# Kernel optimization log

Hardware: AMD Instinct MI355X
Metric: run time of the kernel (lower is better)

Reference implementation:

```python
import jax, jax.numpy as jnp
import numpy as np

# static config (mirrors init_kwargs)
FS = 512          # frame_seqlen
NFPB = 2          # num_frame_per_block
NIB = 3           # num image/action/state blocks
NAPB = 32         # num_action_per_block
NSPB = 1          # num_state_per_block
LOCAL = 4         # local_attn_size (frames)
FIRST = FS
IMGB = NIB * NFPB * FS
ALEN = NIB * NAPB
SLEN = NIB * NSPB
TOTAL = FIRST + IMGB + ALEN + SLEN   # 3683
DIM = 1536
NH = 12
HD = DIM // NH    # 128
EPS = 1e-6


def _build_mask():
    # faithful port of _visualize_attention_mask (the block-sparse pattern)
    m = np.zeros((TOTAL, TOTAL), dtype=bool)
    fi0, fi1 = 0, FIRST
    ib0, ib1 = fi1, fi1 + IMGB
    a0, a1 = ib1, ib1 + ALEN
    s0 = a1
    m[fi0:fi1, fi0:fi1] = True  # first image: self only (sink)
    for b in range(NIB):
        bs = ib0 + b * NFPB * FS
        be = ib0 + (b + 1) * NFPB * FS
        m[bs:be, fi0:fi1] = True                      # sink
        kv = max(ib0, be - LOCAL * FS)                # local window
        m[bs:be, kv:be] = True
        m[bs:be, a0 + b * NAPB:a0 + (b + 1) * NAPB] = True
        m[bs:be, s0 + b * NSPB:s0 + (b + 1) * NSPB] = True
    for b in range(NIB):
        ab0 = a0 + b * NAPB
        ab1 = a0 + (b + 1) * NAPB
        m[ab0:ab1, fi0:fi1] = True
        ibe = ib0 + (b + 1) * NFPB * FS
        kv = max(ib0, ibe - LOCAL * FS)
        m[ab0:ab1, kv:ibe] = True
        m[ab0:ab1, ab0:ab1] = True
        m[ab0:ab1, s0 + b * NSPB:s0 + (b + 1) * NSPB] = True
    for b in range(NIB):
        ss = s0 + b * NSPB
        se = s0 + (b + 1) * NSPB
        m[ss:se, ss:se] = True
    return m

_MASK = jnp.asarray(_build_mask())


def _rms_norm(x, g):
    # WanRMSNorm over full dim, fp32 accumulation
    v = jnp.mean(jnp.square(x.astype(jnp.float32)), axis=-1, keepdims=True)
    return (x.astype(jnp.float32) * jax.lax.rsqrt(v + EPS)).astype(x.dtype) * g


def _rope(x, cos, sin):
    # x: [B,L,n,hd]; pairs are consecutive (..., hd//2, 2)
    B, L, n, d = x.shape
    xp = x.reshape(B, L, n, d // 2, 2)
    xr, xi = xp[..., 0], xp[..., 1]
    c = cos[None, :, None, :]
    s = sin[None, :, None, :]
    yr = xr * c - xi * s
    yi = xr * s + xi * c
    return jnp.stack([yr, yi], axis=-1).reshape(B, L, n, d)


def setup_inputs() -> dict:
    key = jax.random.key(0)
    ks = jax.random.split(key, 16)
    x = jax.random.normal(ks[0], (1, TOTAL, DIM), jnp.float32)

    def mkfreq(k, L):
        ang = jax.random.uniform(k, (L, HD // 2), jnp.float32, 0.0, 2.0 * np.pi)
        return jnp.stack([jnp.cos(ang), jnp.sin(ang)], axis=-1).reshape(L, HD)

    freqs = mkfreq(ks[1], FIRST + IMGB)
    freqs_action = mkfreq(ks[2], ALEN)
    freqs_state = mkfreq(ks[3], SLEN)
    sc = 1.0 / np.sqrt(DIM)
    Wq = jax.random.normal(ks[4], (DIM, DIM), jnp.float32) * sc
    Wk = jax.random.normal(ks[5], (DIM, DIM), jnp.float32) * sc
    Wv = jax.random.normal(ks[6], (DIM, DIM), jnp.float32) * sc
    Wo = jax.random.normal(ks[7], (DIM, DIM), jnp.float32) * sc
    bq = jax.random.normal(ks[8], (DIM,), jnp.float32) * 0.01
    bk = jax.random.normal(ks[9], (DIM,), jnp.float32) * 0.01
    bv = jax.random.normal(ks[10], (DIM,), jnp.float32) * 0.01
    bo = jax.random.normal(ks[11], (DIM,), jnp.float32) * 0.01
    gq = jnp.ones((DIM,), jnp.float32)
    gk = jnp.ones((DIM,), jnp.float32)
    return {"x": x, "freqs": freqs, "freqs_action": freqs_action,
            "freqs_state": freqs_state, "Wq": Wq, "bq": bq, "Wk": Wk, "bk": bk,
            "Wv": Wv, "bv": bv, "Wo": Wo, "bo": bo, "gq": gq, "gk": gk}


def reference(x, freqs, freqs_action, freqs_state, Wq, bq, Wk, bk, Wv, bv, Wo, bo, gq, gk):
    B, L, _ = x.shape
    q = _rms_norm(x @ Wq + bq, gq).reshape(B, L, NH, HD)
    k = _rms_norm(x @ Wk + bk, gk).reshape(B, L, NH, HD)
    v = (x @ Wv + bv).reshape(B, L, NH, HD)
    # full-sequence rope: image freqs then action freqs then state freqs
    f = jnp.concatenate([freqs, freqs_action, freqs_state], axis=0).reshape(L, HD // 2, 2)
    cos, sin = f[..., 0], f[..., 1]
    q = _rope(q, cos, sin)
    k = _rope(k, cos, sin)
    scores = jnp.einsum('bqnd,bknd->bnqk', q, k) / np.sqrt(HD)
    scores = jnp.where(_MASK[None, None], scores, jnp.finfo(scores.dtype).min)
    p = jax.nn.softmax(scores, axis=-1)
    o = jnp.einsum('bnqk,bknd->bqnd', p, v).reshape(B, L, DIM)
    return o @ Wo + bo
```

## Files before the change

### kernel.cpp

```cpp
#include <hip/hip_runtime.h>

#define LSEQ 3683
#define LPAD 3840
#define DIMSZ 1536
#define NHEAD 12
#define HEADD 128
#define SM_SCALE 0.088388347648318447f

typedef unsigned short u16;
typedef unsigned int u32;
typedef __bf16 bf16x8 __attribute__((ext_vector_type(8)));
typedef float f32x4 __attribute__((ext_vector_type(4)));

__device__ __forceinline__ u16 f2b(float f) {
  u32 u = __float_as_uint(f);
  u += 0x7FFFu + ((u >> 16) & 1u);
  return (u16)(u >> 16);
}
__device__ __forceinline__ float b2f(u16 s) {
  return __uint_as_float(((u32)s) << 16);
}
__device__ __forceinline__ int imax(int a, int b) { return a > b ? a : b; }

__device__ __forceinline__ void gl_lds16(const u16* g, u16* l) {
  __builtin_amdgcn_global_load_lds((const __attribute__((address_space(1))) u32*)g,
                                   (__attribute__((address_space(3))) u32*)l,
                                   16, 0, 0);
}

__device__ __forceinline__ int xcd_swz(int orig, int nwg) {
  int q = nwg >> 3, r = nwg & 7;
  int x = orig & 7, l = orig >> 3;
  return (x < r ? x * (q + 1) : r * (q + 1) + (x - r) * q) + l;
}

#define CONV_BLOCKS 5760
__global__ void prep_kernel(const float* __restrict__ x, u16* __restrict__ xb,
                            const float* __restrict__ W0, const float* __restrict__ W1,
                            const float* __restrict__ W2, const float* __restrict__ W3,
                            u16* __restrict__ Wt) {
  __shared__ float tile[32][33];
  int bx = blockIdx.x;
  if (bx < CONV_BLOCKS) {
    long idx = (long)bx * blockDim.x + threadIdx.x;
    long base = idx * 4;
    if (base >= (long)LPAD * DIMSZ) return;
    float4 v;
    if (base < (long)LSEQ * DIMSZ) v = *(const float4*)(x + base);
    else v = make_float4(0.f, 0.f, 0.f, 0.f);
    ushort4 o;
    o.x = f2b(v.x); o.y = f2b(v.y); o.z = f2b(v.z); o.w = f2b(v.w);
    *(ushort4*)(xb + base) = o;
  } else {
    int i = bx - CONV_BLOCKS;
    int z = i / 2304;
    int r = i % 2304;
    int bxx = r % 48, byy = r / 48;
    const float* W = (z == 0) ? W0 : (z == 1) ? W1 : (z == 2) ? W2 : W3;
    u16* dst = Wt + (size_t)z * DIMSZ * DIMSZ;
    int k0 = bxx * 32, n0 = byy * 32;
    int tx = threadIdx.x & 31, ty = threadIdx.x >> 5;
    #pragma unroll
    for (int q = 0; q < 4; q++) {
      int k = k0 + ty + q * 8;
      tile[ty + q * 8][tx] = W[(size_t)k * DIMSZ + n0 + tx];
    }
    __syncthreads();
    #pragma unroll
    for (int q = 0; q < 4; q++) {
      int n = n0 + ty + q * 8;
      dst[(size_t)n * DIMSZ + k0 + tx] = f2b(tile[tx][ty + q * 8]);
    }
  }
}

#define BAR() __builtin_amdgcn_s_barrier()
#define LGK0() asm volatile("s_waitcnt lgkmcnt(0)" ::: "memory")
#define LGK8() asm volatile("s_waitcnt lgkmcnt(8)" ::: "memory")
#define VMC9() asm volatile("s_waitcnt vmcnt(9)" ::: "memory")
#define VMC6() asm volatile("s_waitcnt vmcnt(6)" ::: "memory")
#define VMC3() asm volatile("s_waitcnt vmcnt(3)" ::: "memory")
#define VMC0() asm volatile("s_waitcnt vmcnt(0)" ::: "memory")
#define PRIO1() __builtin_amdgcn_s_setprio(1)
#define PRIO0() __builtin_amdgcn_s_setprio(0)

#define STG_A(buf, q, kt) \
  gl_lds16(gA + (size_t)((q) * 64) * DIMSZ + (kt), &Asg[buf][((q) * 64 + w * 8) * 64]);
#define STG_B(buf, q, kt) \
  gl_lds16(gB + (size_t)((q) * 64) * DIMSZ + (kt), &Bsg[buf][((q) * 64 + w * 8) * 64]);

#define LDA3(buf, mh) { \
  _Pragma("unroll") for (int mf = 0; mf < 3; mf++) { \
    int rb = (wm * 96 + (mh) * 48 + mf * 16) * 64; \
    Ar[mf * 2 + 0] = *(const bf16x8*)&Asg[buf][rb + off0]; \
    Ar[mf * 2 + 1] = *(const bf16x8*)&Asg[buf][rb + off1]; } }
#define LDB3(buf, nh) { \
  _Pragma("unroll") for (int nf = 0; nf < 3; nf++) { \
    int rb = (wn * 96 + (nh) * 48 + nf * 16) * 64; \
    Br[nh][nf * 2 + 0] = *(const bf16x8*)&Bsg[buf][rb + off0]; \
    Br[nh][nf * 2 + 1] = *(const bf16x8*)&Bsg[buf][rb + off1]; } }

#define MFMAQ3(mh, nh) { \
  _Pragma("unroll") for (int mf = 0; mf < 3; mf++) \
    _Pragma("unroll") for (int nf = 0; nf < 3; nf++) { \
      acc[(mh)*3+mf][(nh)*3+nf] = __builtin_amdgcn_mfma_f32_16x16x32_bf16(Ar[mf*2+0], Br[nh][nf*2+0], acc[(mh)*3+mf][(nh)*3+nf], 0, 0, 0); \
      acc[(mh)*3+mf][(nh)*3+nf] = __builtin_amdgcn_mfma_f32_16x16x32_bf16(Ar[mf*2+1], Br[nh][nf*2+1], acc[(mh)*3+mf][(nh)*3+nf], 0, 0, 0); } }

#define GEMM384_BODY() \
  STG_B(0, 0, 0) STG_B(0, 1, 0) STG_B(0, 2, 0) \
  STG_A(0, 0, 0) STG_A(0, 1, 0) STG_A(0, 2, 0) \
  STG_A(0, 3, 0) STG_A(0, 4, 0) STG_A(0, 5, 0) \
  STG_B(1, 0, 64) STG_B(1, 1, 64) STG_B(1, 2, 64) \
  STG_A(1, 0, 64) STG_A(1, 1, 64) STG_A(1, 2, 64) \
  STG_A(1, 3, 64) STG_A(1, 4, 64) STG_A(1, 5, 64) \
  VMC9(); \
  BAR(); \
  for (int i = 0; i < DIMSZ / 64 / 2 - 1; ++i) { \
    int kt2 = (2 * i + 2) * 64; \
    int kt3 = (2 * i + 3) * 64; \
    LDA3(0, 0) LDB3(0, 0) \
    LGK8(); BAR(); LGK0(); \
    PRIO1(); MFMAQ3(0, 0) PRIO0(); \
    BAR(); \
    LDB3(0, 1) \
    BAR(); LGK0(); \
    PRIO1(); MFMAQ3(0, 1) PRIO0(); \
    BAR(); \
    LDA3(0, 1) \
    STG_B(0, 0, kt2) STG_B(0, 1, kt2) STG_B(0, 2, kt2) \
    BAR(); LGK0(); \
    PRIO1(); MFMAQ3(1, 1) PRIO0(); \
    BAR(); \
    STG_A(0, 0, kt2) STG_A(0, 1, kt2) STG_A(0, 2, kt2) \
    VMC6(); BAR(); \
    PRIO1(); MFMAQ3(1, 0) PRIO0(); \
    BAR(); \
    LDA3(1, 0) LDB3(1, 0) \
    STG_A(0, 3, kt2) STG_A(0, 4, kt2) STG_A(0, 5, kt2) \
    LGK8(); BAR(); LGK0(); \
    PRIO1(); MFMAQ3(0, 0) PRIO0(); \
    BAR(); \
    LDB3(1, 1) \
    BAR(); LGK0(); \
    PRIO1(); MFMAQ3(0, 1) PRIO0(); \
    BAR(); \
    LDA3(1, 1) \
    STG_B(1, 0, kt3) STG_B(1, 1, kt3) STG_B(1, 2, kt3) \
    BAR(); LGK0(); \
    PRIO1(); MFMAQ3(1, 1) PRIO0(); \
    BAR(); \
    STG_A(1, 0, kt3) STG_A(1, 1, kt3) STG_A(1, 2, kt3) \
    STG_A(1, 3, kt3) STG_A(1, 4, kt3) STG_A(1, 5, kt3) \
    VMC9(); BAR(); \
    PRIO1(); MFMAQ3(1, 0) PRIO0(); \
    BAR(); \
  } \
  { \
    LDA3(0, 0) LDB3(0, 0) \
    LGK8(); BAR(); LGK0(); \
    PRIO1(); MFMAQ3(0, 0) PRIO0(); \
    BAR(); \
    LDB3(0, 1) \
    BAR(); LGK0(); \
    PRIO1(); MFMAQ3(0, 1) PRIO0(); \
    BAR(); \
    LDA3(0, 1) \
    BAR(); LGK0(); \
    PRIO1(); MFMAQ3(1, 1) PRIO0(); \
    BAR(); \
    VMC0(); BAR(); \
    PRIO1(); MFMAQ3(1, 0) PRIO0(); \
    BAR(); \
    LDA3(1, 0) LDB3(1, 0) \
    LGK8(); BAR(); LGK0(); \
    PRIO1(); MFMAQ3(0, 0) PRIO0(); \
    BAR(); \
    LDB3(1, 1) \
    BAR(); LGK0(); \
    PRIO1(); MFMAQ3(0, 1) PRIO0(); \
    BAR(); \
    LDA3(1, 1) \
    BAR(); LGK0(); \
    PRIO1(); MFMAQ3(1, 1) PRIO0(); \
    MFMAQ3(1, 0) \
  }

__launch_bounds__(512, 2)
__global__ void gemm_qkv384_kernel(const u16* __restrict__ A, const u16* __restrict__ Wt,
                                   const float* __restrict__ bq, const float* __restrict__ bk,
                                   const float* __restrict__ bv,
                                   u16* __restrict__ Qb, u16* __restrict__ Kb,
                                   u16* __restrict__ Vt) {
  __shared__ __align__(16) u16 Asg[2][384 * 64];
  __shared__ __align__(16) u16 Bsg[2][192 * 64];

  int wg = xcd_swz(blockIdx.x, 10 * 24);
  int nt = wg % 24;
  int m0 = (wg / 24) * 384;
  int which = nt >> 3;
  const float* bias = (which == 0) ? bq : (which == 1) ? bk : bv;

  int t = threadIdx.x;
  int lane = t & 63, w = t >> 6;
  int c = lane & 15, g = lane >> 4;
  int wm = w >> 1, wn = w & 1;

  int srow = t >> 3;
  int schunk = ((t & 7) ^ (srow & 7)) * 8;
  const u16* gA = A + (size_t)(m0 + srow) * DIMSZ + schunk;
  const u16* gB = Wt + (size_t)(nt * 192 + srow) * DIMSZ + schunk;

  int off0 = c * 64 + ((g) ^ (c & 7)) * 8;
  int off1 = c * 64 + ((g + 4) ^ (c & 7)) * 8;

  f32x4 acc[6][6];
  f32x4 zero = {0.f, 0.f, 0.f, 0.f};
  #pragma unroll
  for (int am = 0; am < 6; am++)
    #pragma unroll
    for (int an = 0; an < 6; an++) acc[am][an] = zero;
  bf16x8 Ar[6];
  bf16x8 Br[2][6];

  GEMM384_BODY()

  #pragma unroll
  for (int an = 0; an < 6; an++) {
    int ncol = (nt & 7) * 192 + wn * 96 + (an / 3) * 48 + (an % 3) * 16 + c;
    float bvv = bias[ncol];
    #pragma unroll
    for (int am = 0; am < 6; am++) {
      int rowb = m0 + wm * 96 + (am / 3) * 48 + (am % 3) * 16 + 4 * g;
      if (which == 2) {
        ushort4 pv;
        pv.x = f2b(acc[am][an][0] + bvv);
        pv.y = f2b(acc[am][an][1] + bvv);
        pv.z = f2b(acc[am][an][2] + bvv);
        pv.w = f2b(acc[am][an][3] + bvv);
        *(ushort4*)&Vt[(size_t)ncol * LPAD + rowb] = pv;
      } else {
        u16* P = (which == 1) ? Kb : Qb;
        #pragma unroll
        for (int r = 0; r < 4; r++)
          P[(size_t)(rowb + r) * DIMSZ + ncol] = f2b(acc[am][an][r] + bvv);
      }
    }
  }
}

#define LDB3S(buf) { \
  _Pragma("unroll") for (int nf = 0; nf < 3; nf++) { \
    int rb = (wn * 48 + nf * 16) * 64; \
    Br2[nf * 2 + 0] = *(const bf16x8*)&Bsg[buf][rb + off0]; \
    Br2[nf * 2 + 1] = *(const bf16x8*)&Bsg[buf][rb + off1]; } }

#define MFMAQ2(mh) { \
  _Pragma("unroll") for (int mf = 0; mf < 3; mf++) \
    _Pragma("unroll") for (int nf = 0; nf < 3; nf++) { \
      acc2[(mh)*3+mf][nf] = __builtin_amdgcn_mfma_f32_16x16x32_bf16(Ar[mf*2+0], Br2[nf*2+0], acc2[(mh)*3+mf][nf], 0, 0, 0); \
      acc2[(mh)*3+mf][nf] = __builtin_amdgcn_mfma_f32_16x16x32_bf16(Ar[mf*2+1], Br2[nf*2+1], acc2[(mh)*3+mf][nf], 0, 0, 0); } }

__launch_bounds__(512, 2)
__global__ void gemm_out192_kernel(const u16* __restrict__ A, const u16* __restrict__ Bt,
                                   const float* __restrict__ bias, float* __restrict__ outF) {
  __shared__ __align__(16) u16 Asg[2][192 * 64];
  __shared__ __align__(16) u16 Bsg[2][192 * 64];

  int wg = xcd_swz(blockIdx.x, 160);
  int nt = wg & 7;
  int m0 = (wg >> 3) * 192;

  int t = threadIdx.x;
  int lane = t & 63, w = t >> 6;
  int c = lane & 15, g = lane >> 4;
  int wm = w >> 2, wn = w & 3;

  int srow = t >> 3;
  int schunk = ((t & 7) ^ (srow & 7)) * 8;
  const u16* gA = A + (size_t)(m0 + srow) * DIMSZ + schunk;
  const u16* gB = Bt + (size_t)(nt * 192 + srow) * DIMSZ + schunk;

  int off0 = c * 64 + ((g) ^ (c & 7)) * 8;
  int off1 = c * 64 + ((g + 4) ^ (c & 7)) * 8;

  f32x4 acc2[6][3];
  f32x4 zero = {0.f, 0.f, 0.f, 0.f};
  #pragma unroll
  for (int am = 0; am < 6; am++)
    #pragma unroll
    for (int an = 0; an < 3; an++) acc2[am][an] = zero;
  bf16x8 Ar[6];
  bf16x8 Br2[6];

  STG_B(0, 0, 0) STG_B(0, 1, 0) STG_B(0, 2, 0)
  STG_A(0, 0, 0) STG_A(0, 1, 0) STG_A(0, 2, 0)
  STG_B(1, 0, 64) STG_B(1, 1, 64) STG_B(1, 2, 64)
  VMC3();
  BAR();

  for (int i = 0; i < DIMSZ / 64 / 2 - 1; ++i) {
    int ktn1 = (2 * i + 1) * 64;
    int kt2  = (2 * i + 2) * 64;
    int kt3  = (2 * i + 3) * 64;
    LDA3(0, 0) LDB3S(0)
    STG_A(1, 0, ktn1) STG_A(1, 1, ktn1) STG_A(1, 2, ktn1)
    LGK8(); BAR(); LGK0();
    PRIO1(); MFMAQ2(0) PRIO0();
    BAR();
    LDA3(0, 1)
    STG_B(0, 0, kt2) STG_B(0, 1, kt2) STG_B(0, 2, kt2)
    VMC3(); BAR(); LGK0();
    PRIO1(); MFMAQ2(1) PRIO0();
    BAR();
    LDA3(1, 0) LDB3S(1)
    STG_A(0, 0, kt2) STG_A(0, 1, kt2) STG_A(0, 2, kt2)
    LGK8(); BAR(); LGK0();
    PRIO1(); MFMAQ2(0) PRIO0();
    BAR();
    LDA3(1, 1)
    STG_B(1, 0, kt3) STG_B(1, 1, kt3) STG_B(1, 2, kt3)
    VMC3(); BAR(); LGK0();
    PRIO1(); MFMAQ2(1) PRIO0();
    BAR();
  }

  {
    LDA3(0, 0) LDB3S(0)
    STG_A(1, 0, DIMSZ - 64) STG_A(1, 1, DIMSZ - 64) STG_A(1, 2, DIMSZ - 64)
    LGK8(); BAR(); LGK0();
    PRIO1(); MFMAQ2(0) PRIO0();
    BAR();
    LDA3(0, 1)
    VMC0(); BAR(); LGK0();
    PRIO1(); MFMAQ2(1) PRIO0();
    BAR();
    LDA3(1, 0) LDB3S(1)
    LGK8(); BAR(); LGK0();
    PRIO1(); MFMAQ2(0) PRIO0();
    BAR();
    LDA3(1, 1)
    LGK0();
    MFMAQ2(1)
  }

  #pragma unroll
  for (int an = 0; an < 3; an++) {
    int ncol = nt * 192 + wn * 48 + an * 16 + c;
    float bvv = bias[ncol];
    #pragma unroll
    for (int am = 0; am < 6; am++) {
      int rowb = m0 + wm * 96 + (am / 3) * 48 + (am % 3) * 16 + 4 * g;
      #pragma unroll
      for (int r = 0; r < 4; r++) {
        int row = rowb + r;
        if (row < LSEQ) outF[(size_t)row * DIMSZ + ncol] = acc2[am][an][r] + bvv;
      }
    }
  }
}

__launch_bounds__(256)
__global__ void normrope_kernel(u16* __restrict__ Qb, u16* __restrict__ Kb,
                                const float* __restrict__ gq, const float* __restrict__ gk,
                                const float* __restrict__ freqs, const float* __restrict__ freqs_a,
                                const float* __restrict__ freqs_s) {
  int l = blockIdx.x;
  int sel = blockIdx.y;
  u16* P = sel ? Kb : Qb;
  const float* gvec = sel ? gk : gq;
  int t = threadIdx.x;
  u16* row = P + (size_t)l * DIMSZ;
  float xv[6];
  #pragma unroll
  for (int i = 0; i < 3; i++) {
    int p = i * 256 + t;
    ushort2 u = *(const ushort2*)(row + 2 * p);
    xv[2 * i] = b2f(u.x);
    xv[2 * i + 1] = b2f(u.y);
  }
  float ss = 0.f;
  #pragma unroll
  for (int i = 0; i < 6; i++) ss += xv[i] * xv[i];
  #pragma unroll
  for (int d = 32; d; d >>= 1) ss += __shfl_down(ss, d);
  __shared__ float red[4];
  __shared__ float rshare;
  if ((t & 63) == 0) red[t >> 6] = ss;
  __syncthreads();
  if (t == 0) rshare = rsqrtf((red[0] + red[1] + red[2] + red[3]) * (1.0f / DIMSZ) + 1e-6f);
  __syncthreads();
  float rms = rshare;

  const float* f = (l < 3584) ? (freqs + (size_t)l * HEADD)
                : (l < 3680) ? (freqs_a + (size_t)(l - 3584) * HEADD)
                             : (freqs_s + (size_t)(l - 3680) * HEADD);
  #pragma unroll
  for (int i = 0; i < 3; i++) {
    int p = i * 256 + t;
    int j = p & 63;
    float2 csn = *(const float2*)(f + 2 * j);
    float2 gv = *(const float2*)(gvec + 2 * p);
    float xr = xv[2 * i] * rms * gv.x;
    float xi = xv[2 * i + 1] * rms * gv.y;
    ushort2 o;
    o.x = f2b(xr * csn.x - xi * csn.y);
    o.y = f2b(xr * csn.y + xi * csn.x);
    *(ushort2*)(row + 2 * p) = o;
  }
}

#define PSLOT_U16 16640
#define NTAIL 84
__launch_bounds__(256, 2)
__global__ void attn_fused_kernel(const u16* __restrict__ Q, const u16* __restrict__ K,
                                  const u16* __restrict__ Vt, u16* __restrict__ O,
                                  u16* __restrict__ DP, float* __restrict__ Part) {
  __shared__ __align__(16) u16 Ks[2][32 * 136];
  __shared__ __align__(16) u16 Vs[2][128 * 40];
  __shared__ __align__(16) u16 Pl[4][32 * 40];

  int t = threadIdx.x, lane = t & 63, w = t >> 6, g = lane >> 4, c = lane & 15;
  const float c1 = SM_SCALE * 1.44269504088896340f;
  const float c2 = 12.0f * 1.44269504088896340f;

  f32x4 zero = {0.f, 0.f, 0.f, 0.f};
  bf16x8 onesv;
  {
    u16 ob = 0x3F80;
    #pragma unroll
    for (int i = 0; i < 8; i++) onesv[i] = ((const __bf16*)&ob)[0];
  }

  if (blockIdx.x < NTAIL) {
    char* smem = (char*)&Ks[0][0];
    float* Lsum = (float*)(smem + 20608);

    int j = blockIdx.x;
    int bxx = j % 7;
    int h = j / 7;
    int qt, part;
    if (bxx < 3) { qt = 112 + bxx; part = 0; }
    else if (bxx < 6) { qt = 112 + (bxx - 3); part = 1; }
    else { qt = 115; part = 0; }
    int qbase = qt * 32;
    bool heavy = (qt <= 114);

    int S0, E0, S1, E1, S2, E2, S3, E3, niv;
    if (qbase < 3680) {
      int b = (qbase - 3584) >> 5;
      int ibe = 512 + (b + 1) * 1024;
      int kv = imax(512, ibe - 2048);
      S0 = 0; E0 = 512; S1 = kv; E1 = ibe;
      S2 = 3584 + 32 * b; E2 = S2 + 32; S3 = 3680 + b; E3 = S3 + 1; niv = 4;
    } else {
      S0 = 3680; E0 = 3683; S1 = S2 = S3 = 0; E1 = E2 = E3 = 0; niv = 1;
    }
    bool diag = (qbase >= 3680);

    int B0 = S0 & ~31, B1 = S1 & ~31, B2 = S2 & ~31, B3 = S3 & ~31;
    int T1 = (E0 - B0 + 31) >> 5;
    int T2 = T1 + ((niv > 1) ? ((E1 - B1 + 31) >> 5) : 0);
    int T3 = T2 + ((niv > 2) ? ((E2 - B2 + 31) >> 5) : 0);
    int T4 = T3 + ((niv > 3) ? ((E3 - B3 + 31) >> 5) : 0);
    int ntile = T4;

    int rlo = 0, rhi = ntile;
    if (heavy) { int half = (ntile + 1) >> 1; if (part == 0) rhi = half; else rlo = half; }

    auto tile_of = [&](int f, int& k0, int& lo, int& hi) {
      k0 = B0 + (f << 5); lo = S0; hi = E0;
      if (niv > 1 && f >= T1) { k0 = B1 + ((f - T1) << 5); lo = S1; hi = E1; }
      if (niv > 2 && f >= T2) { k0 = B2 + ((f - T2) << 5); lo = S2; hi = E2; }
      if (niv > 3 && f >= T3) { k0 = B3 + ((f - T3) << 5); lo = S3; hi = E3; }
    };

    bf16x8 qf[2][4];
    #pragma unroll
    for (int a = 0; a < 2; a++) {
      const u16* qp = Q + (size_t)(qbase + a * 16 + c) * DIMSZ + h * HEADD + 8 * g;
      #pragma unroll
      for (int s = 0; s < 4; s++) qf[a][s] = *(const bf16x8*)(qp + 32 * s);
    }

    f32x4 acc[2][8];
    f32x4 lacc[2];
    #pragma unroll
    for (int a = 0; a < 2; a++) {
      lacc[a] = zero;
      #pragma unroll
      for (int cc = 0; cc < 8; cc++) acc[a][cc] = zero;
    }

    u16* PwA = (u16*)smem + w * 2560;
    u16* PwB = PwA + 1280;

    bf16x8 kc[2][4], vbuf[8], pa0, pa1;

    auto loadK = [&](int k0) {
      #pragma unroll
      for (int k2 = 0; k2 < 2; k2++) {
        const u16* kp = K + (size_t)(k0 + 16 * k2 + c) * DIMSZ + h * HEADD + 8 * g;
        #pragma unroll
        for (int s = 0; s < 4; s++) kc[k2][s] = *(const bf16x8*)(kp + 32 * s);
      }
    };
    auto loadV = [&](int k0) {
      #pragma unroll
      for (int cc = 0; cc < 8; cc++)
        vbuf[cc] = *(const bf16x8*)(Vt + (size_t)(h * HEADD + cc * 16 + c) * LPAD + k0 + 8 * g);
    };
    auto QKf = [&](f32x4 (&sc)[2][2]) {
      sc[0][0] = zero; sc[0][1] = zero; sc[1][0] = zero; sc[1][1] = zero;
      #pragma unroll
      for (int k2 = 0; k2 < 2; k2++)
        #pragma unroll
        for (int s = 0; s < 4; s++) {
          sc[0][k2] = __builtin_amdgcn_mfma_f32_16x16x32_bf16(qf[0][s], kc[k2][s], sc[0][k2], 0, 0, 0);
          sc[1][k2] = __builtin_amdgcn_mfma_f32_16x16x32_bf16(qf[1][s], kc[k2][s], sc[1][k2], 0, 0, 0);
        }
    };
    auto smstore = [&](f32x4 (&sc)[2][2], int k0, int lo, int hi, u16* Pw) {
      #pragma unroll
      for (int a = 0; a < 2; a++)
        #pragma unroll
        for (int k2 = 0; k2 < 2; k2++) {
          int k = k0 + k2 * 16 + c;
          bool valid = (k >= lo) && (k < hi);
          #pragma unroll
          for (int r = 0; r < 4; r++) {
            float p = __builtin_amdgcn_exp2f(sc[a][k2][r] * c1 - c2);
            bool v = valid;
            if (diag) { int qr = qbase + a * 16 + 4 * g + r; v = v && (k == qr); }
            Pw[(a * 16 + 4 * g + r) * 40 + k2 * 16 + c] = v ? f2b(p) : (u16)0;
          }
        }
    };
    auto readP = [&](u16* Pw) {
      pa0 = *(const bf16x8*)&Pw[c * 40 + 8 * g];
      pa1 = *(const bf16x8*)&Pw[(16 + c) * 40 + 8 * g];
    };
    auto PV = [&]() {
      #pragma unroll
      for (int cc = 0; cc < 8; cc++) {
        acc[0][cc] = __builtin_amdgcn_mfma_f32_16x16x32_bf16(pa0, vbuf[cc], acc[0][cc], 0, 0, 0);
        acc[1][cc] = __builtin_amdgcn_mfma_f32_16x16x32_bf16(pa1, vbuf[cc], acc[1][cc], 0, 0, 0);
      }
      lacc[0] = __builtin_amdgcn_mfma_f32_16x16x32_bf16(pa0, onesv, lacc[0], 0, 0, 0);
      lacc[1] = __builtin_amdgcn_mfma_f32_16x16x32_bf16(pa1, onesv, lacc[1], 0, 0, 0);
    };

    int i = rlo + w;
    if (i < rhi) {
      int ik0, ilo, ihi; tile_of(i, ik0, ilo, ihi);
      loadK(ik0);
      loadV(ik0);
      {
        f32x4 sc[2][2]; QKf(sc);
        smstore(sc, ik0, ilo, ihi, PwA);
      }
      asm volatile("s_waitcnt lgkmcnt(0)" ::: "memory");
      __builtin_amdgcn_sched_barrier(0);
      readP(PwA);
      int nx = i + 4;
      int nk0 = 0, nlo = 0, nhi = 0;
      bool useB = true;
      if (nx < rhi) { tile_of(nx, nk0, nlo, nhi); loadK(nk0); }
      while (nx < rhi) {
        int ck0 = nk0, clo = nlo, chi = nhi;
        f32x4 sc[2][2]; QKf(sc);
        int nn = nx + 4;
        if (nn < rhi) { tile_of(nn, nk0, nlo, nhi); loadK(nk0); }
        u16* Pw = useB ? PwB : PwA;
        smstore(sc, ck0, clo, chi, Pw);
        PV();
        loadV(ck0);
        asm volatile("s_waitcnt lgkmcnt(0)" ::: "memory");
        __builtin_amdgcn_sched_barrier(0);
        readP(Pw);
        useB = !useB;
        i = nx; nx = nn;
      }
      PV();
    }

    __syncthreads();
    float* Oacc = (float*)smem;
    if (w == 0) {
      #pragma unroll
      for (int a = 0; a < 2; a++) {
        #pragma unroll
        for (int cc = 0; cc < 8; cc++)
          #pragma unroll
          for (int r = 0; r < 4; r++)
            Oacc[(a * 16 + 4 * g + r) * 132 + cc * 16 + c] = acc[a][cc][r];
        if (c == 0)
          #pragma unroll
          for (int r = 0; r < 4; r++) Lsum[a * 16 + 4 * g + r] = lacc[a][r];
      }
    }
    __syncthreads();
    #pragma unroll
    for (int ww = 1; ww < 4; ww++) {
      if (w == ww) {
        #pragma unroll
        for (int a = 0; a < 2; a++) {
          #pragma unroll
          for (int cc = 0; cc < 8; cc++)
            #pragma unroll
            for (int r = 0; r < 4; r++)
              Oacc[(a * 16 + 4 * g + r) * 132 + cc * 16 + c] += acc[a][cc][r];
          if (c == 0)
            #pragma unroll
            for (int r = 0; r < 4; r++) Lsum[a * 16 + 4 * g + r] += lacc[a][r];
        }
      }
      __syncthreads();
    }

    int row = t >> 3, c0 = (t & 7) * 16;
    if (heavy) {
      size_t slot = ((size_t)((qt - 112) * 12 + h)) * 2 + part;
      float* P = Part + slot * 4160;
      #pragma unroll
      for (int jj = 0; jj < 16; jj += 4)
        *(float4*)&P[row * 128 + c0 + jj] = *(float4*)&Oacc[row * 132 + c0 + jj];
      if ((t & 7) == 0) P[4096 + row] = Lsum[row];
    } else {
      int orow = qbase + row;
      if (orow < LSEQ) {
        float lsv = Lsum[row];
        float inv = (lsv > 0.f) ? 1.0f / lsv : 0.f;
        u16 tmp[16];
        #pragma unroll
        for (int jj = 0; jj < 16; jj++) tmp[jj] = f2b(Oacc[row * 132 + c0 + jj] * inv);
        u16* op = O + (size_t)orow * DIMSZ + h * HEADD + c0;
        *(uint4*)(op) = *(uint4*)&tmp[0];
        *(uint4*)(op + 8) = *(uint4*)&tmp[8];
      }
    }
    return;
  }

  int bx0 = blockIdx.x - NTAIL;
  int j = (bx0 & 7) * 138 + (bx0 >> 3);
  int h = j / 92;
  int u = j % 92;
  int qbase, part, nparts, fb;
  if (u < 4) { fb = -1; qbase = u * 128; part = 0; nparts = 1; }
  else if (u < 28) { int v = u - 4; fb = 0; qbase = 512 + (v / 3) * 128; part = v % 3; nparts = 3; }
  else if (u < 60) { int v = u - 28; fb = 1; qbase = 1536 + (v / 4) * 128; part = v % 4; nparts = 4; }
  else { int v = u - 60; fb = 2; qbase = 2560 + (v / 4) * 128; part = v % 4; nparts = 4; }

  int S0, E0, S1, E1, S2, E2, S3, E3, niv;
  if (fb < 0) { S0 = 0; E0 = 512; S1 = E1 = S2 = E2 = S3 = E3 = 0; niv = 1; }
  else {
    int be = 512 + (fb + 1) * 1024;
    int kv = imax(512, be - 2048);
    S0 = 0; E0 = 512; S1 = kv; E1 = be;
    S2 = 3584 + 32 * fb; E2 = S2 + 32; S3 = 3680 + fb; E3 = S3 + 1; niv = 4;
  }
  int B0 = S0 & ~31, B1 = S1 & ~31, B2 = S2 & ~31, B3 = S3 & ~31;
  int T1 = (E0 - B0 + 31) >> 5;
  int T2 = T1 + ((niv > 1) ? ((E1 - B1 + 31) >> 5) : 0);
  int T3 = T2 + ((niv > 2) ? ((E2 - B2 + 31) >> 5) : 0);
  int T4 = T3 + ((niv > 3) ? ((E3 - B3 + 31) >> 5) : 0);
  int ntile = T4;
  int rlo = (ntile * part) / nparts, rhi = (ntile * (part + 1)) / nparts;

  auto tile_of = [&](int f, int& k0, int& lo, int& hi) {
    k0 = B0 + (f << 5); lo = S0; hi = E0;
    if (niv > 1 && f >= T1) { k0 = B1 + ((f - T1) << 5); lo = S1; hi = E1; }
    if (niv > 2 && f >= T2) { k0 = B2 + ((f - T2) << 5); lo = S2; hi = E2; }
    if (niv > 3 && f >= T3) { k0 = B3 + ((f - T3) << 5); lo = S3; hi = E3; }
  };

  const u16* kgp = K + (size_t)(t >> 3) * DIMSZ + h * HEADD + 8 * (t & 7);
  int kds = (t >> 3) * 136 + 8 * (t & 7);
  const u16* vgp = Vt + ((size_t)h * HEADD + (t >> 1)) * LPAD + 16 * (t & 1);
  int vds = (t >> 1) * 40 + 16 * (t & 1);

  uint4 sk0, sk1, sv0, sv1;
  auto stage_load = [&](int k0) {
    const u16* kp = kgp + (size_t)k0 * DIMSZ;
    sk0 = *(const uint4*)(kp);
    sk1 = *(const uint4*)(kp + 64);
    sv0 = *(const uint4*)(vgp + k0);
    sv1 = *(const uint4*)(vgp + k0 + 8);
  };
  auto stage_write = [&](int buf) {
    *(uint4*)&Ks[buf][kds] = sk0;
    *(uint4*)&Ks[buf][kds + 64] = sk1;
    *(uint4*)&Vs[buf][vds] = sv0;
    *(uint4*)&Vs[buf][vds + 8] = sv1;
  };

  int qrow0 = qbase + 32 * w;
  bf16x8 qf[2][4];
  #pragma unroll
  for (int a = 0; a < 2; a++) {
    const u16* qp = Q + (size_t)(qrow0 + a * 16 + c) * DIMSZ + h * HEADD + 8 * g;
    #pragma unroll
    for (int s = 0; s < 4; s++) qf[a][s] = *(const bf16x8*)(qp + 32 * s);
  }

  f32x4 acc[2][8];
  f32x4 lacc[2];
  #pragma unroll
  for (int a = 0; a < 2; a++) {
    lacc[a] = zero;
    #pragma unroll
    for (int cc = 0; cc < 8; cc++) acc[a][cc] = zero;
  }

  u16* Pw = &Pl[w][0];
  __bf16* Pwh = (__bf16*)Pw;

  {
    int k0, lo, hi; tile_of(rlo, k0, lo, hi);
    stage_load(k0);
    stage_write(0);
  }
  __syncthreads();
  int cur = 0;

  for (int tt = rlo; tt < rhi; ++tt) {
    int ck0, clo, chi; tile_of(tt, ck0, clo, chi);
    bool pre = (tt + 1 < rhi);
    if (pre) { int nk0, nl, nh; tile_of(tt + 1, nk0, nl, nh); stage_load(nk0); }

    f32x4 sc[2][2];
    sc[0][0] = zero; sc[0][1] = zero; sc[1][0] = zero; sc[1][1] = zero;
    #pragma unroll
    for (int k2 = 0; k2 < 2; k2++)
      #pragma unroll
      for (int s = 0; s < 4; s++) {
        bf16x8 kf = *(const bf16x8*)&Ks[cur][(16 * k2 + c) * 136 + 32 * s + 8 * g];
        sc[0][k2] = __builtin_amdgcn_mfma_f32_16x16x32_bf16(qf[0][s], kf, sc[0][k2], 0, 0, 0);
        sc[1][k2] = __builtin_amdgcn_mfma_f32_16x16x32_bf16(qf[1][s], kf, sc[1][k2], 0, 0, 0);
      }

    if (ck0 >= clo && ck0 + 32 <= chi) {
      #pragma unroll
      for (int a = 0; a < 2; a++)
        #pragma unroll
        for (int k2 = 0; k2 < 2; k2++)
          #pragma unroll
          for (int r = 0; r < 4; r++) {
            float p = __builtin_amdgcn_exp2f(sc[a][k2][r] * c1 - c2);
            Pwh[(a * 16 + 4 * g + r) * 40 + k2 * 16 + c] = (__bf16)p;
          }
    } else {
      #pragma unroll
      for (int a = 0; a < 2; a++)
        #pragma unroll
        for (int k2 = 0; k2 < 2; k2++) {
          int k = ck0 + k2 * 16 + c;
          bool valid = (k >= clo) && (k < chi);
          #pragma unroll
          for (int r = 0; r < 4; r++) {
            float p = __builtin_amdgcn_exp2f(sc[a][k2][r] * c1 - c2);
            Pwh[(a * 16 + 4 * g + r) * 40 + k2 * 16 + c] = valid ? (__bf16)p : (__bf16)0.0f;
          }
        }
    }
    asm volatile("s_waitcnt lgkmcnt(0)" ::: "memory");
    __builtin_amdgcn_sched_barrier(0);

    bf16x8 pa0 = *(const bf16x8*)&Pw[c * 40 + 8 * g];
    bf16x8 pa1 = *(const bf16x8*)&Pw[(16 + c) * 40 + 8 * g];

    #pragma unroll
    for (int cc = 0; cc < 8; cc++) {
      bf16x8 vf = *(const bf16x8*)&Vs[cur][(cc * 16 + c) * 40 + 8 * g];
      acc[0][cc] = __builtin_amdgcn_mfma_f32_16x16x32_bf16(pa0, vf, acc[0][cc], 0, 0, 0);
      acc[1][cc] = __builtin_amdgcn_mfma_f32_16x16x32_bf16(pa1, vf, acc[1][cc], 0, 0, 0);
    }
    lacc[0] = __builtin_amdgcn_mfma_f32_16x16x32_bf16(pa0, onesv, lacc[0], 0, 0, 0);
    lacc[1] = __builtin_amdgcn_mfma_f32_16x16x32_bf16(pa1, onesv, lacc[1], 0, 0, 0);

    if (pre) stage_write(cur ^ 1);
    __syncthreads();
    cur ^= 1;
  }

  if (nparts == 1) {
    float inv[2][4];
    #pragma unroll
    for (int a = 0; a < 2; a++)
      #pragma unroll
      for (int r = 0; r < 4; r++) inv[a][r] = (lacc[a][r] > 0.f) ? 1.0f / lacc[a][r] : 0.f;
    #pragma unroll
    for (int a = 0; a < 2; a++)
      #pragma unroll
      for (int cc = 0; cc < 8; cc++)
        #pragma unroll
        for (int r = 0; r < 4; r++) {
          int row = qrow0 + a * 16 + 4 * g + r;
          O[(size_t)row * DIMSZ + h * HEADD + cc * 16 + c] = f2b(acc[a][cc][r] * inv[a][r]);
        }
  } else {
    int qb = (qbase - 512 - fb * 1024) >> 7;
    int sbase = (fb == 0) ? 0 : (fb == 1 ? 288 : 672);
    int slot = sbase + (qb * 12 + h) * nparts + part;
    u16* DPs = DP + (size_t)slot * PSLOT_U16;
    float* lout = (float*)(DPs + 16384);
    #pragma unroll
    for (int a = 0; a < 2; a++) {
      #pragma unroll
      for (int cc = 0; cc < 8; cc++)
        #pragma unroll
        for (int r = 0; r < 4; r++)
          DPs[(32 * w + a * 16 + 4 * g + r) * 128 + cc * 16 + c] = f2b(acc[a][cc][r]);
      if (c == 0)
        #pragma unroll
        for (int r = 0; r < 4; r++) lout[32 * w + a * 16 + 4 * g + r] = lacc[a][r];
    }
  }
}

__launch_bounds__(256)
__global__ void attn_merge_kernel(const u16* __restrict__ DP, const float* __restrict__ Part,
                                  u16* __restrict__ O) {
  int bx = blockIdx.x, h = blockIdx.y;
  int T = threadIdx.x;
  if (bx < 24) {
    int qi = bx;
    int fb = qi >> 3, qb = qi & 7;
    int nparts = (fb == 0) ? 3 : 4;
    int sbase = (fb == 0) ? 0 : (fb == 1 ? 288 : 672);
    int slot0 = sbase + (qb * 12 + h) * nparts;
    int qbase = 512 + fb * 1024 + qb * 128;
    int row = T >> 1, c0 = 64 * (T & 1);

    float sum[64];
    #pragma unroll
    for (int j = 0; j < 64; j++) sum[j] = 0.f;
    float l = 0.f;
    for (int p = 0; p < nparts; p++) {
      const u16* S = DP + (size_t)(slot0 + p) * PSLOT_U16;
      l += ((const float*)(S + 16384))[row];
      #pragma unroll
      for (int j = 0; j < 64; j += 8) {
        uint4 v = *(const uint4*)&S[row * 128 + c0 + j];
        const u16* pv = (const u16*)&v;
        #pragma unroll
        for (int q = 0; q < 8; q++) sum[j + q] += b2f(pv[q]);
      }
    }
    float inv = (l > 0.f) ? 1.0f / l : 0.f;
    u16 tmp[64];
    #pragma unroll
    for (int j = 0; j < 64; j++) tmp[j] = f2b(sum[j] * inv);
    u16* op = O + (size_t)(qbase + row) * DIMSZ + h * HEADD + c0;
    #pragma unroll
    for (int j = 0; j < 64; j += 8) *(uint4*)(op + j) = *(uint4*)&tmp[j];
  } else {
    int b = bx - 24;
    const float* A = Part + ((size_t)(b * 12 + h)) * 2 * 4160;
    const float* B = A + 4160;
    int row = T >> 3, c0 = (T & 7) * 16;
    float l = A[4096 + row] + B[4096 + row];
    float inv = (l > 0.f) ? 1.0f / l : 0.f;
    int orow = 3584 + b * 32 + row;
    u16 tmp[16];
    #pragma unroll
    for (int jj = 0; jj < 16; jj += 4) {
      float4 va = *(const float4*)&A[row * 128 + c0 + jj];
      float4 vb = *(const float4*)&B[row * 128 + c0 + jj];
      tmp[jj + 0] = f2b((va.x + vb.x) * inv);
      tmp[jj + 1] = f2b((va.y + vb.y) * inv);
      tmp[jj + 2] = f2b((va.z + vb.z) * inv);
      tmp[jj + 3] = f2b((va.w + vb.w) * inv);
    }
    u16* op = O + (size_t)orow * DIMSZ + h * HEADD + c0;
    *(uint4*)(op) = *(uint4*)&tmp[0];
    *(uint4*)(op + 8) = *(uint4*)&tmp[8];
  }
}

extern "C" void kernel_launch(void* const* d_in, const int* in_sizes, int n_in,
                              void* d_out, int out_size, void* d_ws, size_t ws_size,
                              hipStream_t stream) {
  (void)in_sizes; (void)n_in; (void)out_size; (void)ws_size;
  const float* x       = (const float*)d_in[0];
  const float* freqs   = (const float*)d_in[1];
  const float* freqs_a = (const float*)d_in[2];
  const float* freqs_s = (const float*)d_in[3];
  const float* Wq = (const float*)d_in[4];
  const float* bq = (const float*)d_in[5];
  const float* Wk = (const float*)d_in[6];
  const float* bk = (const float*)d_in[7];
  const float* Wv = (const float*)d_in[8];
  const float* bv = (const float*)d_in[9];
  const float* Wo = (const float*)d_in[10];
  const float* bo = (const float*)d_in[11];
  const float* gq = (const float*)d_in[12];
  const float* gk = (const float*)d_in[13];
  float* out = (float*)d_out;

  char* ws = (char*)d_ws;
  size_t off = 0;
  auto alloc = [&](size_t bytes) -> void* {
    void* p = ws + off;
    off += (bytes + 255) & ~(size_t)255;
    return p;
  };
  u16* xb   = (u16*)alloc((size_t)LPAD * DIMSZ * 2);
  u16* Wt   = (u16*)alloc((size_t)4 * DIMSZ * DIMSZ * 2);
  u16* Qb   = (u16*)alloc((size_t)LPAD * DIMSZ * 2);
  u16* Kb   = (u16*)alloc((size_t)LPAD * DIMSZ * 2);
  u16* Vt   = (u16*)alloc((size_t)DIMSZ * LPAD * 2);
  u16* Ob   = (u16*)alloc((size_t)LPAD * DIMSZ * 2);
  u16* DP   = (u16*)alloc((size_t)1056 * PSLOT_U16 * 2);
  float* PartT = (float*)alloc((size_t)3 * 12 * 2 * 4160 * 4);

  prep_kernel<<<dim3(CONV_BLOCKS + 9216), 256, 0, stream>>>(x, xb, Wq, Wk, Wv, Wo, Wt);

  gemm_qkv384_kernel<<<dim3(240), 512, 0, stream>>>(xb, Wt, bq, bk, bv, Qb, Kb, Vt);

  normrope_kernel<<<dim3(LSEQ, 2), 256, 0, stream>>>(Qb, Kb, gq, gk, freqs, freqs_a, freqs_s);

  attn_fused_kernel<<<dim3(NTAIL + 1104), 256, 0, stream>>>(Qb, Kb, Vt, Ob, DP, PartT);
  attn_merge_kernel<<<dim3(27, 12), 256, 0, stream>>>(DP, PartT, Ob);

  gemm_out192_kernel<<<dim3(160), 512, 0, stream>>>(Ob, Wt + 3 * (size_t)DIMSZ * DIMSZ, bo, out);
}
```

Before: 216.9 us.

## Replace software-pipelined attention tile loop with simple loop and split V loads

The double-buffered P/K/V prefetch pipeline in the sparse attention tile loop is replaced by a straightforward per-tile loop. Each iteration loads K, computes QK, stores P to LDS, then loads V in two halves of four fragments with the PV MFMAs interleaved. This likely lowers register pressure (vbuf halved, no prefetched K) and simplifies the schedule. The cost is that global-load latency is no longer hidden behind the previous tile's compute.

```diff
diff --git a/kernel.cpp b/kernel.cpp
--- a/kernel.cpp
+++ b/kernel.cpp
@@ -492,9 +492,8 @@
     }
 
     u16* PwA = (u16*)smem + w * 2560;
-    u16* PwB = PwA + 1280;
-
-    bf16x8 kc[2][4], vbuf[8], pa0, pa1;
+
+    bf16x8 kc[2][4], vbuf[4], pa0, pa1;
 
     auto loadK = [&](int k0) {
       #pragma unroll
@@ -504,10 +503,10 @@
         for (int s = 0; s < 4; s++) kc[k2][s] = *(const bf16x8*)(kp + 32 * s);
       }
     };
-    auto loadV = [&](int k0) {
-      #pragma unroll
-      for (int cc = 0; cc < 8; cc++)
-        vbuf[cc] = *(const bf16x8*)(Vt + (size_t)(h * HEADD + cc * 16 + c) * LPAD + k0 + 8 * g);
+    auto loadV4 = [&](int k0, int hh) {
+      #pragma unroll
+      for (int cc = 0; cc < 4; cc++)
+        vbuf[cc] = *(const bf16x8*)(Vt + (size_t)(h * HEADD + (hh * 4 + cc) * 16 + c) * LPAD + k0 + 8 * g);
     };
     auto QKf = [&](f32x4 (&sc)[2][2]) {
       sc[0][0] = zero; sc[0][1] = zero; sc[1][0] = zero; sc[1][1] = zero;
@@ -535,52 +534,27 @@
           }
         }
     };
-    auto readP = [&](u16* Pw) {
-      pa0 = *(const bf16x8*)&Pw[c * 40 + 8 * g];
-      pa1 = *(const bf16x8*)&Pw[(16 + c) * 40 + 8 * g];
+    auto PV4 = [&](int hh) {
+      #pragma unroll
+      for (int cc = 0; cc < 4; cc++) {
+        acc[0][hh * 4 + cc] = __builtin_amdgcn_mfma_f32_16x16x32_bf16(pa0, vbuf[cc], acc[0][hh * 4 + cc], 0, 0, 0);
+        acc[1][hh * 4 + cc] = __builtin_amdgcn_mfma_f32_16x16x32_bf16(pa1, vbuf[cc], acc[1][hh * 4 + cc], 0, 0, 0);
+      }
     };
-    auto PV = [&]() {
-      #pragma unroll
-      for (int cc = 0; cc < 8; cc++) {
-        acc[0][cc] = __builtin_amdgcn_mfma_f32_16x16x32_bf16(pa0, vbuf[cc], acc[0][cc], 0, 0, 0);
-        acc[1][cc] = __builtin_amdgcn_mfma_f32_16x16x32_bf16(pa1, vbuf[cc], acc[1][cc], 0, 0, 0);
-      }
+
+    for (int i = rlo + w; i < rhi; i += 4) {
+      int ik0, ilo, ihi; tile_of(i, ik0, ilo, ihi);
+      loadK(ik0);
+      f32x4 sc[2][2]; QKf(sc);
+      smstore(sc, ik0, ilo, ihi, PwA);
+      asm volatile("s_waitcnt lgkmcnt(0)" ::: "memory");
+      __builtin_amdgcn_sched_barrier(0);
+      pa0 = *(const bf16x8*)&PwA[c * 40 + 8 * g];
+      pa1 = *(const bf16x8*)&PwA[(16 + c) * 40 + 8 * g];
+      loadV4(ik0, 0); PV4(0);
+      loadV4(ik0, 1); PV4(1);
       lacc[0] = __builtin_amdgcn_mfma_f32_16x16x32_bf16(pa0, onesv, lacc[0], 0, 0, 0);
       lacc[1] = __builtin_amdgcn_mfma_f32_16x16x32_bf16(pa1, onesv, lacc[1], 0, 0, 0);
-    };
-
-    int i = rlo + w;
-    if (i < rhi) {
-      int ik0, ilo, ihi; tile_of(i, ik0, ilo, ihi);
-      loadK(ik0);
-      loadV(ik0);
-      {
-        f32x4 sc[2][2]; QKf(sc);
-        smstore(sc, ik0, ilo, ihi, PwA);
-      }
-      asm volatile("s_waitcnt lgkmcnt(0)" ::: "memory");
-      __builtin_amdgcn_sched_barrier(0);
-      readP(PwA);
-      int nx = i + 4;
-      int nk0 = 0, nlo = 0, nhi = 0;
-      bool useB = true;
-      if (nx < rhi) { tile_of(nx, nk0, nlo, nhi); loadK(nk0); }
-      while (nx < rhi) {
-        int ck0 = nk0, clo = nlo, chi = nhi;
-        f32x4 sc[2][2]; QKf(sc);
-        int nn = nx + 4;
-        if (nn < rhi) { tile_of(nn, nk0, nlo, nhi); loadK(nk0); }
-        u16* Pw = useB ? PwB : PwA;
-        smstore(sc, ck0, clo, chi, Pw);
-        PV();
-        loadV(ck0);
-        asm volatile("s_waitcnt lgkmcnt(0)" ::: "memory");
-        __builtin_amdgcn_sched_barrier(0);
-        readP(Pw);
-        useB = !useB;
-        i = nx; nx = nn;
-      }
-      PV();
     }
 
     __syncthreads();
```

Result: no change. 217.3 us (+0.2%).
